# Kernel optimization log

Measured on AMD Instinct MI355X. Metric: run time of the kernel, lower is better.

## Reference

```python
import jax, jax.numpy as jnp
import numpy as np

C, H2, E, SQ, SK, HW = 256, 256, 512, 2048, 64, 256

def setup_inputs() -> dict:
    key = jax.random.key(0)
    ks = jax.random.split(key, 12)
    s = 0.05
    return {
        "Z": jax.random.normal(ks[0], (C, HW, HW), jnp.float32),
        "Q": jax.random.normal(ks[1], (SQ, 3), jnp.float32),
        "q_z": jax.random.normal(ks[2], (SQ, C), jnp.float32),
        "r": jax.random.uniform(ks[3], (SQ, SK, 2), jnp.float32) * (HW - 2),
        "w1": jax.random.normal(ks[4], (H2, 2), jnp.float32) * s,
        "b1": jnp.zeros((H2,), jnp.float32),
        "w2": jax.random.normal(ks[5], (H2, 3), jnp.float32) * s,
        "b2": jnp.zeros((H2,), jnp.float32),
        "in_proj_w": jax.random.normal(ks[6], (3 * E, E), jnp.float32) * s,
        "in_proj_b": jnp.zeros((3 * E,), jnp.float32),
        "out_proj_w": jax.random.normal(ks[7], (E, E), jnp.float32) * s,
        "out_proj_b": jnp.zeros((E,), jnp.float32),
        "num_heads": 8,
    }

def bilinear_interpolation_3d(Z, x, y):
    # Z: [c, H, W]; x, y: [N] float coords. Faithful to torch: .int() trunc (coords >= 0)
    c = Z.shape[0]
    x1 = x.astype(jnp.int32)
    y1 = y.astype(jnp.int32)
    x2 = x1 + 1
    y2 = y1 + 1
    Q11 = Z[:, x1, y1]  # [c, N]
    Q12 = Z[:, x1, y2]
    Q21 = Z[:, x2, y1]
    Q22 = Z[:, x2, y2]
    dx = x - x1
    dy = y - y1
    R1 = Q11 * (1 - dx) + Q21 * dx
    R2 = Q12 * (1 - dx) + Q22 * dx
    interp = R1 * (1 - dy) + R2 * dy  # [c, N]
    # faithful to the original: raw row-major reshape (NOT a transpose)
    return jnp.reshape(interp, (-1, c))

def reference(Z, Q, q_z, r, w1, b1, w2, b2, in_proj_w, in_proj_b, out_proj_w, out_proj_b, num_heads):
    size_q, size_k, _ = r.shape
    qr = r.reshape(-1, 2)
    Zr = bilinear_interpolation_3d(Z, qr[:, 0], qr[:, 1])
    Zr = Zr.reshape(size_q, size_k, -1)  # [sq, sk, c]
    r_proj = r @ w1.T + b1               # [sq, sk, h2]
    key = jnp.concatenate([Zr, r_proj], axis=2)  # [sq, sk, E]
    value = key
    q_proj = Q @ w2.T + b2               # [sq, h2]
    query = jnp.concatenate([q_z, q_proj], axis=1)  # [sq, E]
    E_ = query.shape[1]
    hd = E_ // num_heads
    # torch MultiheadAttention in-projection
    ql = query @ in_proj_w[:E_].T + in_proj_b[:E_]              # [sq, E]
    kl = key @ in_proj_w[E_:2 * E_].T + in_proj_b[E_:2 * E_]    # [sq, sk, E]
    vl = value @ in_proj_w[2 * E_:].T + in_proj_b[2 * E_:]
    qh = ql.reshape(size_q, num_heads, hd)
    kh = kl.reshape(size_q, size_k, num_heads, hd)
    vh = vl.reshape(size_q, size_k, num_heads, hd)
    scores = jnp.einsum('bhd,bkhd->bhk', qh, kh) / jnp.sqrt(jnp.asarray(hd, qh.dtype))
    attn = jax.nn.softmax(scores, axis=-1)  # [sq, h, sk]
    out = jnp.einsum('bhk,bkhd->bhd', attn, vh).reshape(size_q, E_)
    out = out @ out_proj_w.T + out_proj_b
    return jnp.concatenate([q_z, out], axis=1)  # [sq, c + E]
```

## Files before the change

### kernel.cpp

```cpp
#include <hip/hip_runtime.h>


typedef _Float16 half8 __attribute__((ext_vector_type(8)));
typedef _Float16 half4v __attribute__((ext_vector_type(4)));
typedef _Float16 half2v __attribute__((ext_vector_type(2)));
typedef float f32x4 __attribute__((ext_vector_type(4)));

#define O_QRY   1048576u
#define O_WCT   2097152u
#define O_MT    4194304u
#define O_U     6291456u
#define O_G     14680064u
#define O_ZT    23068672u
#define O_ZR    39845888u
#define O_F32   73400320u

__global__ __launch_bounds__(256) void k_pre(
    const float* __restrict__ Z, const float* __restrict__ ipw,
    const float* __restrict__ opw, const float* __restrict__ q_z,
    const float* __restrict__ Qm, const float* __restrict__ w2,
    const float* __restrict__ b2, const float* __restrict__ ipb,
    const float* __restrict__ opb,
    _Float16* __restrict__ wsh, float* __restrict__ bu, float* __restrict__ b_eff)
{
    __shared__ __align__(16) unsigned char sbuf[33792];
    int b = blockIdx.x, t = threadIdx.x;

    if (b < 2048) {
        float (*sT)[33] = (float(*)[33])sbuf;
        int x = b >> 3, yt = (b & 7) * 32;
#pragma unroll
        for (int i = 0; i < 8; ++i) {
            int g = i * 256 + t;
            int c = g >> 3, y = (g & 7) * 4;
            float4 v = *(const float4*)(Z + (size_t)c * 65536 + x * 256 + yt + y);
            sT[c][y] = v.x; sT[c][y + 1] = v.y; sT[c][y + 2] = v.z; sT[c][y + 3] = v.w;
        }
        __syncthreads();
        _Float16* Zt = wsh + O_ZT;
        int c4 = (t & 63) * 4;
#pragma unroll
        for (int i = 0; i < 8; ++i) {
            int y = (t >> 6) * 8 + i;
            half4v o;
#pragma unroll
            for (int j = 0; j < 4; ++j) o[j] = (_Float16)sT[c4 + j][y];
            *(half4v*)(Zt + ((size_t)(x * 256 + yt + y)) * 256 + c4) = o;
        }
    } else if (b < 3072) {
        int e4 = ((b - 2048) * 256 + t) * 4;
        int q = e4 >> 9, j = e4 & 511;
        half4v o;
        if (j < 256) {
            float4 v = *(const float4*)(q_z + q * 256 + j);
            o[0] = (_Float16)v.x; o[1] = (_Float16)v.y;
            o[2] = (_Float16)v.z; o[3] = (_Float16)v.w;
        } else {
            float q0 = Qm[q * 3], q1 = Qm[q * 3 + 1], q2 = Qm[q * 3 + 2];
#pragma unroll
            for (int u = 0; u < 4; ++u) {
                int m = j - 256 + u;
                o[u] = (_Float16)(q0 * w2[m * 3] + q1 * w2[m * 3 + 1] + q2 * w2[m * 3 + 2] + b2[m]);
            }
        }
        *(half4v*)(wsh + O_QRY + e4) = o;
    } else if (b < 4096) {
        int isMt = (b >= 3584);
        int b2_ = b - (isMt ? 3584 : 3072);
        int h = b2_ >> 6, jt = (b2_ >> 3) & 7, lt = b2_ & 7;
        _Float16 (*sAm)[72] = (_Float16(*)[72])sbuf;
        _Float16 (*sBn)[72] = (_Float16(*)[72])(sbuf + 9216);
        int j0 = jt * 64, l0 = lt * 64;
        int dd = t >> 4, c4 = (t & 15) * 4;
#pragma unroll
        for (int ii = 0; ii < 4; ++ii) {
            int d = ii * 16 + dd;
            if (!isMt) {
                float4 k4 = *(const float4*)(ipw + (size_t)(512 + h * 64 + d) * 512 + j0 + c4);
                float4 q4 = *(const float4*)(ipw + (size_t)(h * 64 + d) * 512 + l0 + c4);
                sAm[c4 + 0][d] = (_Float16)(0.125f * k4.x);
                sAm[c4 + 1][d] = (_Float16)(0.125f * k4.y);
                sAm[c4 + 2][d] = (_Float16)(0.125f * k4.z);
                sAm[c4 + 3][d] = (_Float16)(0.125f * k4.w);
                sBn[c4 + 0][d] = (_Float16)q4.x;
                sBn[c4 + 1][d] = (_Float16)q4.y;
                sBn[c4 + 2][d] = (_Float16)q4.z;
                sBn[c4 + 3][d] = (_Float16)q4.w;
            } else {
                int e = ii * 16 + dd;
                float4 o4 = *(const float4*)(opw + (size_t)(l0 + e) * 512 + h * 64 + c4);
                half4v ov;
                ov[0] = (_Float16)o4.x; ov[1] = (_Float16)o4.y;
                ov[2] = (_Float16)o4.z; ov[3] = (_Float16)o4.w;
                *(half4v*)&sAm[e][c4] = ov;
                float4 v4 = *(const float4*)(ipw + (size_t)(1024 + h * 64 + d) * 512 + j0 + c4);
                sBn[c4 + 0][d] = (_Float16)v4.x;
                sBn[c4 + 1][d] = (_Float16)v4.y;
                sBn[c4 + 2][d] = (_Float16)v4.z;
                sBn[c4 + 3][d] = (_Float16)v4.w;
            }
        }
        __syncthreads();
        int w = t >> 6, l = t & 63;
        int arow = l & 15, kg = (l >> 4) << 3;
        f32x4 acc[4] = {};
#pragma unroll
        for (int kk = 0; kk < 64; kk += 32) {
            half8 a = *(const half8*)&sAm[w * 16 + arow][kk + kg];
#pragma unroll
            for (int nt = 0; nt < 4; ++nt) {
                half8 bb = *(const half8*)&sBn[nt * 16 + arow][kk + kg];
                acc[nt] = __builtin_amdgcn_mfma_f32_16x16x32_f16(a, bb, acc[nt], 0, 0, 0);
            }
        }
        int rg = (l >> 4) << 2;
        if (!isMt) {
            _Float16* Wc = wsh + O_WCT;
#pragma unroll
            for (int nt = 0; nt < 4; ++nt)
#pragma unroll
                for (int v = 0; v < 4; ++v)
                    Wc[(size_t)(h * 512 + j0 + w * 16 + rg + v) * 512 + l0 + nt * 16 + arow] =
                        (_Float16)acc[nt][v];
        } else {
            _Float16* Mt = wsh + O_MT;
#pragma unroll
            for (int nt = 0; nt < 4; ++nt)
#pragma unroll
                for (int v = 0; v < 4; ++v)
                    Mt[(size_t)(l0 + w * 16 + rg + v) * 4096 + h * 512 + j0 + nt * 16 + arow] =
                        (_Float16)acc[nt][v];
        }
    } else if (b < 4112) {
        int c = (b - 4096) * 256 + t;
        int h = c >> 9, j = c & 511;
        float s = 0.f;
#pragma unroll 4
        for (int d = 0; d < 64; ++d)
            s += ipb[512 + (h << 6) + d] * ipw[(size_t)(512 + (h << 6) + d) * 512 + j];
        bu[c] = 0.125f * s;
    } else {
        int e = (b - 4112) * 4 + (t >> 6), l = t & 63;
        const float* worow = opw + (size_t)e * 512;
        float s = 0.f;
#pragma unroll
        for (int i = 0; i < 8; ++i)
            s += ipb[1024 + l + 64 * i] * worow[l + 64 * i];
#pragma unroll
        for (int mm = 1; mm < 64; mm <<= 1) s += __shfl_xor(s, mm, 64);
        if (l == 0) b_eff[e] = s + opb[e];
    }
}

__global__ __launch_bounds__(256, 4) void k_mid(
    const float* __restrict__ r, _Float16* __restrict__ wsh,
    const float* __restrict__ bu)
{
    __shared__ __align__(16) unsigned char smem[33792];
    int b = blockIdx.x, t = threadIdx.x, w = t >> 6, l = t & 63;

    if (b < 512) {
        _Float16 (*sA)[264] = (_Float16(*)[264])smem;
        const _Float16* A = wsh + O_QRY;
        const _Float16* B = wsh + O_WCT;
        _Float16* U = wsh + O_U;
        int q0 = (b & 31) * 64;
        int colb = (b >> 5) * 256 + w * 64;
        f32x4 acc[4][4] = {};
        int arow = l & 15, kg = (l >> 4) << 3;
#pragma unroll
        for (int half = 0; half < 2; ++half) {
#pragma unroll
            for (int i = 0; i < 8; ++i) {
                int e = i * 2048 + t * 8;
                *(half8*)&sA[e >> 8][e & 255] =
                    *(const half8*)(A + (size_t)(q0 + (e >> 8)) * 512 + half * 256 + (e & 255));
            }
            __syncthreads();
#pragma unroll 2
            for (int kk = 0; kk < 256; kk += 32) {
                half8 a[4], bb[4];
#pragma unroll
                for (int mt = 0; mt < 4; ++mt) a[mt] = *(const half8*)&sA[mt * 16 + arow][kk + kg];
#pragma unroll
                for (int nt = 0; nt < 4; ++nt)
                    bb[nt] = *(const half8*)(B + (size_t)(colb + nt * 16 + arow) * 512 + half * 256 + kk + kg);
#pragma unroll
                for (int mt = 0; mt < 4; ++mt)
#pragma unroll
                    for (int nt = 0; nt < 4; ++nt)
                        acc[mt][nt] = __builtin_amdgcn_mfma_f32_16x16x32_f16(a[mt], bb[nt], acc[mt][nt], 0, 0, 0);
            }
            __syncthreads();
        }
#pragma unroll
        for (int mt = 0; mt < 4; ++mt)
#pragma unroll
            for (int nt = 0; nt < 4; ++nt)
#pragma unroll
                for (int v = 0; v < 4; ++v) {
                    int row = q0 + mt * 16 + ((l >> 4) << 2) + v;
                    int col = colb + nt * 16 + arow;
                    U[(size_t)row * 4096 + col] = (_Float16)(acc[mt][nt][v] + bu[col]);
                }
    } else {
        float (*sT)[33] = (float(*)[33])smem;
        const _Float16* Zt = wsh + O_ZT;
        _Float16* Zr = wsh + O_ZR;
        int pb = b - 512;
        const float2* r2 = (const float2*)r;
#pragma unroll 2
        for (int i = 0; i < 8; ++i) {
            int ptl = w * 8 + i;
            float2 rv = r2[pb * 32 + ptl];
            int x1 = (int)rv.x, y1 = (int)rv.y;
            float dx = rv.x - (float)x1, dy = rv.y - (float)y1;
            float w11 = (1.f - dx) * (1.f - dy), w21 = dx * (1.f - dy);
            float w12 = (1.f - dx) * dy,         w22 = dx * dy;
            const _Float16* base = Zt + ((size_t)(x1 * 256 + y1)) * 256;
#pragma unroll
            for (int cg = 0; cg < 2; ++cg) {
                int c = cg * 128 + l * 2;
                half2v z11 = *(const half2v*)(base + c);
                half2v z12 = *(const half2v*)(base + 256 + c);
                half2v z21 = *(const half2v*)(base + 65536 + c);
                half2v z22 = *(const half2v*)(base + 65536 + 256 + c);
                sT[c][ptl]     = w11 * (float)z11[0] + w21 * (float)z21[0]
                               + w12 * (float)z12[0] + w22 * (float)z22[0];
                sT[c + 1][ptl] = w11 * (float)z11[1] + w21 * (float)z21[1]
                               + w12 * (float)z12[1] + w22 * (float)z22[1];
            }
        }
        __syncthreads();
        int ch0 = t >> 2, colc = (t & 3) * 8;
#pragma unroll
        for (int g = 0; g < 4; ++g) {
            int ch = g * 64 + ch0;
            half8 o;
#pragma unroll
            for (int j = 0; j < 8; ++j) o[j] = (_Float16)sT[ch][colc + j];
            *(half8*)(Zr + (size_t)ch * 131072 + pb * 32 + colc) = o;
        }
    }
}

__global__ __launch_bounds__(512, 2) void k_main(
    const _Float16* __restrict__ Zr, const float* __restrict__ r,
    const float* __restrict__ w1, const float* __restrict__ b1,
    const _Float16* __restrict__ U, _Float16* __restrict__ G)
{
    __shared__ __align__(16) _Float16 sKey[64][520];
    __shared__ __align__(16) _Float16 sU[8][520];
    __shared__ float sP[512];
    __shared__ float sP2[512];
    __shared__ __align__(16) _Float16 sA16[16][72];

    int q = blockIdx.x;
    int t = threadIdx.x, w = t >> 6, l = t & 63;
    int ch = q >> 3, s8 = q & 7;

    for (int i = t; i < 576; i += 512) ((unsigned*)sA16)[i] = 0u;

    const _Float16* src = Zr + ((size_t)ch * 2048 + s8 * 256) * 64;
#pragma unroll
    for (int i = 0; i < 4; ++i) {
        int e = i * 4096 + t * 8;
        int k = e >> 8, col = e & 255;
        int colS = (((col >> 3) ^ (k >> 3)) << 3);
        *(half8*)&sKey[k][colS] = *(const half8*)(src + e);
    }
    {
        int e = t * 8;
        *(half8*)&sU[e >> 9][e & 511] = *(const half8*)(U + (size_t)q * 4096 + e);
    }
    {
        int m = t & 255, half = t >> 8;
        float w10 = w1[2 * m], w11 = w1[2 * m + 1], b1m = b1[m];
        const float2* r2q = (const float2*)r + (size_t)q * 64;
#pragma unroll 8
        for (int i = 0; i < 32; ++i) {
            int k = half * 32 + i;
            float2 rv = r2q[k];
            int col = 256 + m;
            int colS = ((((col >> 3) ^ (k >> 3)) << 3)) + (col & 7);
            sKey[k][colS] = (_Float16)(rv.x * w10 + rv.y * w11 + b1m);
        }
    }
    __syncthreads();

    {
        f32x4 acc = {};
        int arow = l & 15, kg = (l >> 4) << 3;
        int wm = w & 3, khalf = (w >> 2) << 8;
        int k = wm * 16 + arow;
        int sw = (k >> 3) & 7;
        const _Float16* krow = &sKey[k][0];
        const _Float16* br = &sU[l & 7][khalf + kg];
#pragma unroll
        for (int kk = 0; kk < 256; kk += 32) {
            int col = khalf + kk + kg;
            half8 av = *(const half8*)(krow + ((((col >> 3) ^ sw) << 3)));
            acc = __builtin_amdgcn_mfma_f32_16x16x32_f16(
                av, *(const half8*)(br + kk), acc, 0, 0, 0);
        }
        if ((l & 15) < 8) {
            int h = l & 15, krow0 = wm * 16 + ((l >> 4) << 2);
            float* dst = (w < 4) ? sP : sP2;
#pragma unroll
            for (int v = 0; v < 4; ++v) dst[(h << 6) + krow0 + v] = acc[v];
        }
    }
    __syncthreads();

    {
        float v = sP[t] + sP2[t];
        float mx = v;
#pragma unroll
        for (int mm = 1; mm < 64; mm <<= 1) mx = fmaxf(mx, __shfl_xor(mx, mm, 64));
        float e = __expf(v - mx);
        float sm = e;
#pragma unroll
        for (int mm = 1; mm < 64; mm <<= 1) sm += __shfl_xor(sm, mm, 64);
        sA16[w][l] = (_Float16)(e / sm);
    }
    __syncthreads();

    {
        f32x4 acc[4] = {};
        int arow = l & 15, kq = (l >> 4) << 3;
        int sw0 = kq >> 3, sw1 = 4 + (kq >> 3);
        half8 a0 = *(const half8*)&sA16[arow][kq];
        half8 a1 = *(const half8*)&sA16[arow][32 + kq];
#pragma unroll
        for (int nt = 0; nt < 4; ++nt) {
            int n0 = (w << 6) + (nt << 4);
            int colb_ = n0 + arow;
            int cg = colb_ >> 3, co = colb_ & 7;
            int c0 = ((cg ^ sw0) << 3) + co;
            int c1 = ((cg ^ sw1) << 3) + co;
            half8 b0, b1f;
#pragma unroll
            for (int jj = 0; jj < 8; ++jj) b0[jj] = sKey[kq + jj][c0];
            acc[nt] = __builtin_amdgcn_mfma_f32_16x16x32_f16(a0, b0, acc[nt], 0, 0, 0);
#pragma unroll
            for (int jj = 0; jj < 8; ++jj) b1f[jj] = sKey[32 + kq + jj][c1];
            acc[nt] = __builtin_amdgcn_mfma_f32_16x16x32_f16(a1, b1f, acc[nt], 0, 0, 0);
        }
        if (l < 32) {
            int rgrp = (l >> 4) << 2;
#pragma unroll
            for (int nt = 0; nt < 4; ++nt) {
                int n0 = (w << 6) + (nt << 4);
#pragma unroll
                for (int v = 0; v < 4; ++v)
                    sU[rgrp + v][n0 + arow] = (_Float16)acc[nt][v];
            }
        }
    }
    __syncthreads();

    {
        int c = t * 8;
        *(half8*)(G + (size_t)q * 4096 + c) = *(const half8*)&sU[c >> 9][c & 511];
    }
}

__global__ __launch_bounds__(256) void k_final(
    const _Float16* __restrict__ G, const _Float16* __restrict__ Mt,
    const float* __restrict__ b_eff, const float* __restrict__ qz,
    float* __restrict__ out)
{
    __shared__ __align__(16) _Float16 sA[32][520];
    int rb = blockIdx.x, cb = blockIdx.y;
    int q0 = rb * 32;
    int t = threadIdx.x, w = t >> 6, l = t & 63;

    if (cb == 0) {
#pragma unroll
        for (int i = 0; i < 8; ++i) {
            int idx4 = i * 256 + t;
            int row = idx4 >> 6, c = (idx4 & 63) << 2;
            *(float4*)&out[(size_t)(q0 + row) * 768 + c] =
                *(const float4*)&qz[(size_t)(q0 + row) * 256 + c];
        }
    }

    f32x4 acc[2][2] = {};
    int arow = l & 15, kg = (l >> 4) << 3;
    int e0 = cb * 128 + (w << 5);
    for (int c = 0; c < 8; ++c) {
#pragma unroll
        for (int i = 0; i < 8; ++i) {
            int e = i * 2048 + t * 8;
            *(half8*)&sA[e >> 9][e & 511] =
                *(const half8*)(G + (size_t)(q0 + (e >> 9)) * 4096 + c * 512 + (e & 511));
        }
        __syncthreads();
#pragma unroll 4
        for (int kk = 0; kk < 512; kk += 32) {
            half8 a[2], bb[2];
#pragma unroll
            for (int nt = 0; nt < 2; ++nt)
                bb[nt] = *(const half8*)(Mt + (size_t)(e0 + nt * 16 + arow) * 4096 + c * 512 + kk + kg);
#pragma unroll
            for (int mt = 0; mt < 2; ++mt) {
                a[mt] = *(const half8*)&sA[mt * 16 + arow][kk + kg];
#pragma unroll
                for (int nt = 0; nt < 2; ++nt)
                    acc[mt][nt] = __builtin_amdgcn_mfma_f32_16x16x32_f16(a[mt], bb[nt], acc[mt][nt], 0, 0, 0);
            }
        }
        __syncthreads();
    }
#pragma unroll
    for (int mt = 0; mt < 2; ++mt)
#pragma unroll
        for (int nt = 0; nt < 2; ++nt)
#pragma unroll
            for (int v = 0; v < 4; ++v) {
                int row = q0 + mt * 16 + ((l >> 4) << 2) + v;
                int ecol = e0 + nt * 16 + arow;
                out[(size_t)row * 768 + 256 + ecol] = acc[mt][nt][v] + b_eff[ecol];
            }
}

extern "C" void kernel_launch(void* const* d_in, const int* in_sizes, int n_in,
                              void* d_out, int out_size, void* d_ws, size_t ws_size,
                              hipStream_t stream) {
    const float* Z          = (const float*)d_in[0];
    const float* Qm         = (const float*)d_in[1];
    const float* q_z        = (const float*)d_in[2];
    const float* r          = (const float*)d_in[3];
    const float* w1         = (const float*)d_in[4];
    const float* b1         = (const float*)d_in[5];
    const float* w2         = (const float*)d_in[6];
    const float* b2         = (const float*)d_in[7];
    const float* in_proj_w  = (const float*)d_in[8];
    const float* in_proj_b  = (const float*)d_in[9];
    const float* out_proj_w = (const float*)d_in[10];
    const float* out_proj_b = (const float*)d_in[11];
    float* out = (float*)d_out;

    _Float16* wsh = (_Float16*)d_ws;
    _Float16* Mt    = wsh + O_MT;
    _Float16* U     = wsh + O_U;
    _Float16* G     = wsh + O_G;
    _Float16* Zr    = wsh + O_ZR;
    float*    bu    = (float*)(wsh + O_F32);
    float*    b_eff = bu + 4096;

    k_pre<<<4240, 256, 0, stream>>>(Z, in_proj_w, out_proj_w, q_z, Qm, w2, b2,
                                    in_proj_b, out_proj_b, wsh, bu, b_eff);
    k_mid<<<4608, 256, 0, stream>>>(r, wsh, bu);
    k_main<<<2048, 512, 0, stream>>>(Zr, r, w1, b1, U, G);
    k_final<<<dim3(64, 4), 256, 0, stream>>>(G, Mt, b_eff, q_z, out);
}
```

Measured before the change: 271.9 us.

## Retile k_mid GEMM to smaller tiles and batch gather blocks over 64 points

The U-projection GEMM in k_mid now uses 32-row tiles with 128-wide K chunks. This doubles the GEMM block count and shrinks shared memory, so the launch bound can rise to 5 blocks per CU. The bilinear gather blocks now each handle 64 points in two passes and write 128-byte contiguous chunks of Zr. The padded transpose buffer is replaced with an XOR-swizzled layout to avoid bank conflicts. In exchange, each GEMM block reloads B from global memory more often and takes more syncs.

Result: slower. 284.9 us (+4.8%).

```diff
diff --git a/kernel.cpp b/kernel.cpp
--- a/kernel.cpp
+++ b/kernel.cpp
@@ -152,41 +152,41 @@
     }
 }
 
-__global__ __launch_bounds__(256, 4) void k_mid(
+__global__ __launch_bounds__(256, 5) void k_mid(
     const float* __restrict__ r, _Float16* __restrict__ wsh,
     const float* __restrict__ bu)
 {
-    __shared__ __align__(16) unsigned char smem[33792];
+    __shared__ __align__(16) unsigned char smem[32768];
     int b = blockIdx.x, t = threadIdx.x, w = t >> 6, l = t & 63;
 
-    if (b < 512) {
-        _Float16 (*sA)[264] = (_Float16(*)[264])smem;
+    if (b < 1024) {
+        _Float16 (*sA)[136] = (_Float16(*)[136])smem;
         const _Float16* A = wsh + O_QRY;
         const _Float16* B = wsh + O_WCT;
         _Float16* U = wsh + O_U;
-        int q0 = (b & 31) * 64;
-        int colb = (b >> 5) * 256 + w * 64;
-        f32x4 acc[4][4] = {};
+        int q0 = (b & 63) * 32;
+        int colb = (b >> 6) * 256 + w * 64;
+        f32x4 acc[2][4] = {};
         int arow = l & 15, kg = (l >> 4) << 3;
 #pragma unroll
-        for (int half = 0; half < 2; ++half) {
-#pragma unroll
-            for (int i = 0; i < 8; ++i) {
+        for (int s = 0; s < 4; ++s) {
+#pragma unroll
+            for (int i = 0; i < 2; ++i) {
                 int e = i * 2048 + t * 8;
-                *(half8*)&sA[e >> 8][e & 255] =
-                    *(const half8*)(A + (size_t)(q0 + (e >> 8)) * 512 + half * 256 + (e & 255));
+                *(half8*)&sA[e >> 7][e & 127] =
+                    *(const half8*)(A + (size_t)(q0 + (e >> 7)) * 512 + s * 128 + (e & 127));
             }
             __syncthreads();
-#pragma unroll 2
-            for (int kk = 0; kk < 256; kk += 32) {
-                half8 a[4], bb[4];
-#pragma unroll
-                for (int mt = 0; mt < 4; ++mt) a[mt] = *(const half8*)&sA[mt * 16 + arow][kk + kg];
+#pragma unroll
+            for (int kk = 0; kk < 128; kk += 32) {
+                half8 a[2], bb[4];
+#pragma unroll
+                for (int mt = 0; mt < 2; ++mt) a[mt] = *(const half8*)&sA[mt * 16 + arow][kk + kg];
 #pragma unroll
                 for (int nt = 0; nt < 4; ++nt)
-                    bb[nt] = *(const half8*)(B + (size_t)(colb + nt * 16 + arow) * 512 + half * 256 + kk + kg);
-#pragma unroll
-                for (int mt = 0; mt < 4; ++mt)
+                    bb[nt] = *(const half8*)(B + (size_t)(colb + nt * 16 + arow) * 512 + s * 128 + kk + kg);
+#pragma unroll
+                for (int mt = 0; mt < 2; ++mt)
 #pragma unroll
                     for (int nt = 0; nt < 4; ++nt)
                         acc[mt][nt] = __builtin_amdgcn_mfma_f32_16x16x32_f16(a[mt], bb[nt], acc[mt][nt], 0, 0, 0);
@@ -194,7 +194,7 @@
             __syncthreads();
         }
 #pragma unroll
-        for (int mt = 0; mt < 4; ++mt)
+        for (int mt = 0; mt < 2; ++mt)
 #pragma unroll
             for (int nt = 0; nt < 4; ++nt)
 #pragma unroll
@@ -204,42 +204,58 @@
                     U[(size_t)row * 4096 + col] = (_Float16)(acc[mt][nt][v] + bu[col]);
                 }
     } else {
-        float (*sT)[33] = (float(*)[33])smem;
+        float (*sT)[32] = (float(*)[32])smem;
         const _Float16* Zt = wsh + O_ZT;
         _Float16* Zr = wsh + O_ZR;
-        int pb = b - 512;
+        int pb = b - 1024;
         const float2* r2 = (const float2*)r;
+        int ch0 = t >> 2, colc = (t & 3) * 8;
+        half8 keep[4];
+
+#pragma unroll
+        for (int hp = 0; hp < 2; ++hp) {
 #pragma unroll 2
-        for (int i = 0; i < 8; ++i) {
-            int ptl = w * 8 + i;
-            float2 rv = r2[pb * 32 + ptl];
-            int x1 = (int)rv.x, y1 = (int)rv.y;
-            float dx = rv.x - (float)x1, dy = rv.y - (float)y1;
-            float w11 = (1.f - dx) * (1.f - dy), w21 = dx * (1.f - dy);
-            float w12 = (1.f - dx) * dy,         w22 = dx * dy;
-            const _Float16* base = Zt + ((size_t)(x1 * 256 + y1)) * 256;
-#pragma unroll
-            for (int cg = 0; cg < 2; ++cg) {
-                int c = cg * 128 + l * 2;
-                half2v z11 = *(const half2v*)(base + c);
-                half2v z12 = *(const half2v*)(base + 256 + c);
-                half2v z21 = *(const half2v*)(base + 65536 + c);
-                half2v z22 = *(const half2v*)(base + 65536 + 256 + c);
-                sT[c][ptl]     = w11 * (float)z11[0] + w21 * (float)z21[0]
-                               + w12 * (float)z12[0] + w22 * (float)z22[0];
-                sT[c + 1][ptl] = w11 * (float)z11[1] + w21 * (float)z21[1]
-                               + w12 * (float)z12[1] + w22 * (float)z22[1];
-            }
-        }
-        __syncthreads();
-        int ch0 = t >> 2, colc = (t & 3) * 8;
-#pragma unroll
-        for (int g = 0; g < 4; ++g) {
-            int ch = g * 64 + ch0;
-            half8 o;
-#pragma unroll
-            for (int j = 0; j < 8; ++j) o[j] = (_Float16)sT[ch][colc + j];
-            *(half8*)(Zr + (size_t)ch * 131072 + pb * 32 + colc) = o;
+            for (int i = 0; i < 8; ++i) {
+                int ptl = w * 8 + i;
+                float2 rv = r2[pb * 64 + hp * 32 + ptl];
+                int x1 = (int)rv.x, y1 = (int)rv.y;
+                float dx = rv.x - (float)x1, dy = rv.y - (float)y1;
+                float w11 = (1.f - dx) * (1.f - dy), w21 = dx * (1.f - dy);
+                float w12 = (1.f - dx) * dy,         w22 = dx * dy;
+                const _Float16* base = Zt + ((size_t)(x1 * 256 + y1)) * 256;
+#pragma unroll
+                for (int cg = 0; cg < 2; ++cg) {
+                    int c = cg * 128 + l * 2;
+                    half2v z11 = *(const half2v*)(base + c);
+                    half2v z12 = *(const half2v*)(base + 256 + c);
+                    half2v z21 = *(const half2v*)(base + 65536 + c);
+                    half2v z22 = *(const half2v*)(base + 65536 + 256 + c);
+                    float v0 = w11 * (float)z11[0] + w21 * (float)z21[0]
+                             + w12 * (float)z12[0] + w22 * (float)z22[0];
+                    float v1 = w11 * (float)z11[1] + w21 * (float)z21[1]
+                             + w12 * (float)z12[1] + w22 * (float)z22[1];
+                    sT[c][ptl ^ (c & 31)] = v0;
+                    sT[c + 1][ptl ^ ((c + 1) & 31)] = v1;
+                }
+            }
+            __syncthreads();
+#pragma unroll
+            for (int g = 0; g < 4; ++g) {
+                int ch = g * 64 + ch0;
+                int x31 = ch & 31;
+                half8 o;
+#pragma unroll
+                for (int j = 0; j < 8; ++j)
+                    o[j] = (_Float16)sT[ch][(colc + j) ^ x31];
+                if (hp == 0) {
+                    keep[g] = o;
+                } else {
+                    _Float16* dst = Zr + (size_t)ch * 131072 + pb * 64 + colc;
+                    *(half8*)dst = keep[g];
+                    *(half8*)(dst + 32) = o;
+                }
+            }
+            if (hp == 0) __syncthreads();
         }
     }
 }
@@ -451,7 +467,7 @@
 
     k_pre<<<4240, 256, 0, stream>>>(Z, in_proj_w, out_proj_w, q_z, Qm, w2, b2,
                                     in_proj_b, out_proj_b, wsh, bu, b_eff);
-    k_mid<<<4608, 256, 0, stream>>>(r, wsh, bu);
+    k_mid<<<3072, 256, 0, stream>>>(r, wsh, bu);
     k_main<<<2048, 512, 0, stream>>>(Zr, r, w1, b1, U, G);
     k_final<<<dim3(64, 4), 256, 0, stream>>>(G, Mt, b_eff, q_z, out);
 }
```
